# Kernel optimization log

Hardware: AMD Instinct MI355X
Metric: run time of the kernel (lower is better)

Reference implementation:

```python
import jax, jax.numpy as jnp
import numpy as np

NUM_USERS = 50000
NUM_ITEMS = 40000
EMB = 64
NNZ = 2_000_000
BATCH = 1024


def setup_inputs() -> dict:
    key = jax.random.key(0)
    ks = jax.random.split(key, 10)
    graph_rows = jax.random.randint(ks[0], (NNZ,), 0, NUM_USERS, dtype=jnp.int32)
    graph_cols = jax.random.randint(ks[1], (NNZ,), 0, NUM_ITEMS, dtype=jnp.int32)
    graph_vals = jax.random.uniform(ks[2], (NNZ,), dtype=jnp.float32)
    Wq = jax.random.normal(ks[3], (2 * EMB, NUM_ITEMS), dtype=jnp.float32) * 0.01
    bq = jnp.zeros((2 * EMB,), jnp.float32)
    Wp = jax.random.normal(ks[4], (NUM_ITEMS, EMB), dtype=jnp.float32) * 0.01
    bp = jnp.zeros((NUM_ITEMS,), jnp.float32)
    user = jax.random.randint(ks[5], (BATCH,), 0, NUM_USERS, dtype=jnp.int32)
    x = (jax.random.uniform(ks[6], (BATCH, NUM_ITEMS)) < 0.02).astype(jnp.float32)
    eps = jax.random.normal(ks[7], (NUM_USERS, EMB), dtype=jnp.float32)
    return dict(graph_vals=graph_vals, Wq=Wq, bq=bq, Wp=Wp, bp=bp, x=x,
                eps=eps, graph_rows=graph_rows, graph_cols=graph_cols, user=user)


def reference(graph_vals, Wq, bq, Wp, bp, x, eps, graph_rows, graph_cols, user):
    # ---- encode: single SpMM  h = Graph @ Wq^T + bq   (dropout off / eval mode)
    # gather item rows of Wq^T per nonzero, scale, scatter-add into users
    gathered = graph_vals[:, None] * Wq.T[graph_cols]          # [nnz, 2E]
    h = jax.ops.segment_sum(gathered, graph_rows, num_segments=NUM_USERS) + bq  # [U, 2E]
    mu, logvar = h[:, :EMB], h[:, EMB:]                        # [U, E] each
    # ---- reparameterize: z = mu + eps * exp(0.5*logvar)
    z = mu + eps * jnp.exp(0.5 * logvar)
    # ---- decode batch users: single Linear(E -> I)
    zb = z[user]                                               # [B, E]
    recon = zb @ Wp.T + bp                                     # [B, I]
    # ---- Mult-VAE ELBO (anneal = 1.0)
    log_sm = jax.nn.log_softmax(recon, axis=-1)
    recon_loss = -jnp.mean(jnp.sum(log_sm * x, axis=-1))
    mu_b, lv_b = mu[user], logvar[user]
    kl_loss = -0.5 * jnp.mean(jnp.sum(1.0 + lv_b - mu_b * mu_b - jnp.exp(lv_b), axis=-1))
    return jnp.stack([recon_loss, kl_loss])  # [2]: (recon_loss, KL_loss)
```

## Files before the change

kernel.cpp:

```cpp
#include <hip/hip_runtime.h>
#include <cstdint>

#define NUM_USERS 50000
#define NUM_ITEMS 40000
#define EMB 64
#define NNZ_E 2000000
#define BATCH 1024
#define NCH 625
#define CAP 131072
#define INF_I 0x7fffffff

typedef __attribute__((ext_vector_type(8))) short short8;
typedef __attribute__((ext_vector_type(4))) float float4v;

__device__ __forceinline__ unsigned short f2bf(float f) {
    union { float f; unsigned u; } x; x.f = f;
    unsigned r = x.u + 0x7fffu + ((x.u >> 16) & 1u);
    return (unsigned short)(r >> 16);
}
__device__ __forceinline__ float bf2f(unsigned short s) {
    return __uint_as_float(((unsigned)s) << 16);
}

__global__ void k_init(int* __restrict__ map, int* __restrict__ cnt, float* __restrict__ scal) {
    int t = blockIdx.x * blockDim.x + threadIdx.x;
    if (t < NUM_USERS) map[t] = INF_I;
    if (t < BATCH) cnt[t] = 0;
    if (t < 4) scal[t] = 0.f;
}

__global__ void k_map(const int* __restrict__ user, int* __restrict__ map) {
    int i = blockIdx.x * blockDim.x + threadIdx.x;
    if (i < BATCH) atomicMin(&map[user[i]], i);
}

__global__ __launch_bounds__(256) void k_prep(const float* __restrict__ Wq,
                                              const float* __restrict__ Wp,
                                              const int* __restrict__ rows,
                                              const int* __restrict__ map,
                                              unsigned short* __restrict__ WqT,
                                              unsigned short* __restrict__ WpBf,
                                              int* __restrict__ cnt) {
    __shared__ float t[128][33];
    const int bid = blockIdx.x;
    const int tid = threadIdx.x;
    if (bid < 1250) {
        const int jb = bid * 32;
        for (int idx = tid; idx < 4096; idx += 256) {
            int d = idx >> 5, c = idx & 31;
            t[d][c] = Wq[(size_t)d * NUM_ITEMS + jb + c];
        }
        __syncthreads();
        for (int idx = tid; idx < 4096; idx += 256) {
            int j = idx >> 7, d = idx & 127;
            WqT[(size_t)(jb + j) * 128 + d] = f2bf(t[d][j]);
        }
    } else if (bid < 3750) {
        const int e0 = ((bid - 1250) * 256 + tid) * 4;
        float4 w = *(const float4*)&Wp[e0];
        ushort4 o;
        o.x = f2bf(w.x); o.y = f2bf(w.y); o.z = f2bf(w.z); o.w = f2bf(w.w);
        *(ushort4*)&WpBf[e0] = o;
    } else {
        const int e = (bid - 3750) * 256 + tid;
        if (e < NNZ_E) {
            int s = map[rows[e]];
            if (s != INF_I) atomicAdd(&cnt[s], 1);
        }
    }
}

__global__ __launch_bounds__(1024) void k_scan(const int* __restrict__ cnt,
                                               int* __restrict__ off, int* __restrict__ cur) {
    __shared__ int s[1024];
    const int t = threadIdx.x;
    const int c = cnt[t];
    s[t] = c; __syncthreads();
    for (int d = 1; d < 1024; d <<= 1) {
        int v = (t >= d) ? s[t - d] : 0;
        __syncthreads();
        s[t] += v;
        __syncthreads();
    }
    int inc = s[t];
    off[t + 1] = inc;
    cur[t] = inc - c;
    if (t == 0) off[0] = 0;
}

__global__ __launch_bounds__(256) void k_scatter(const int* __restrict__ rows,
                                                 const int* __restrict__ cols,
                                                 const float* __restrict__ vals,
                                                 const int* __restrict__ map,
                                                 int* __restrict__ cur,
                                                 int2* __restrict__ compact) {
    const int e = blockIdx.x * 256 + threadIdx.x;
    if (e >= NNZ_E) return;
    int s = map[rows[e]];
    if (s == INF_I) return;
    int pos = atomicAdd(&cur[s], 1);
    if (pos < CAP) compact[pos] = make_int2(cols[e], __float_as_int(vals[e]));
}

__global__ __launch_bounds__(128) void k_hz(const int* __restrict__ user,
                                            const int* __restrict__ map,
                                            const int* __restrict__ off,
                                            const int2* __restrict__ compact,
                                            const unsigned short* __restrict__ WqT,
                                            const float* __restrict__ bq,
                                            const float* __restrict__ eps,
                                            unsigned short* __restrict__ zbBf,
                                            float* __restrict__ scal) {
    __shared__ float sh[128];
    const int i = blockIdx.x;
    const int tid = threadIdx.x;
    const int u = user[i];
    const int s = map[u];
    const int b = off[s], eN = off[s + 1];
    float acc = 0.f;
    int e = b;
    int2 cv = (e < eN) ? compact[e] : make_int2(0, 0);
    while (e < eN) {
        int2 nx = (e + 1 < eN) ? compact[e + 1] : make_int2(0, 0);
        float w = bf2f(WqT[(size_t)cv.x * 128 + tid]);
        acc = fmaf(__int_as_float(cv.y), w, acc);
        cv = nx; e++;
    }
    sh[tid] = acc + bq[tid];
    __syncthreads();
    if (tid < 64) {
        float mu = sh[tid];
        float lv = sh[tid + 64];
        float z = mu + eps[(size_t)u * EMB + tid] * __expf(0.5f * lv);
        zbBf[i * EMB + tid] = f2bf(z);
        float kl = 1.0f + lv - mu * mu - __expf(lv);
        #pragma unroll
        for (int o = 32; o; o >>= 1) kl += __shfl_down(kl, o);
        if (tid == 0) atomicAdd(&scal[1], kl);
    }
}

__global__ __launch_bounds__(256) void k_gemm(const unsigned short* __restrict__ zbBf,
                                              const unsigned short* __restrict__ WpBf,
                                              const float* __restrict__ bp,
                                              const float* __restrict__ x,
                                              float* __restrict__ part) {
    const int tid = threadIdx.x;
    const int wid = tid >> 6, lane = tid & 63;
    const int l15 = lane & 15, quad = lane >> 4;
    const int jb = blockIdx.x * 64;
    const int ibase = blockIdx.y * 128 + wid * 32;

    short8 af[2][2], bf[4][2];
    #pragma unroll
    for (int mt = 0; mt < 2; mt++) {
        const unsigned short* pa = zbBf + (size_t)(ibase + mt * 16 + l15) * EMB + quad * 8;
        af[mt][0] = *(const short8*)pa;
        af[mt][1] = *(const short8*)(pa + 32);
    }
    #pragma unroll
    for (int nt = 0; nt < 4; nt++) {
        const unsigned short* pb = WpBf + (size_t)(jb + nt * 16 + l15) * EMB + quad * 8;
        bf[nt][0] = *(const short8*)pb;
        bf[nt][1] = *(const short8*)(pb + 32);
    }
    float4v acc[2][4];
    #pragma unroll
    for (int mt = 0; mt < 2; mt++)
        #pragma unroll
        for (int nt = 0; nt < 4; nt++)
            acc[mt][nt] = (float4v){0.f, 0.f, 0.f, 0.f};
    #pragma unroll
    for (int kh = 0; kh < 2; kh++)
        #pragma unroll
        for (int mt = 0; mt < 2; mt++)
            #pragma unroll
            for (int nt = 0; nt < 4; nt++)
                acc[mt][nt] = __builtin_amdgcn_mfma_f32_16x16x32_bf16(
                    af[mt][kh], bf[nt][kh], acc[mt][nt], 0, 0, 0);

    float bpv[4];
    #pragma unroll
    for (int nt = 0; nt < 4; nt++) bpv[nt] = bp[jb + nt * 16 + l15];

    #pragma unroll
    for (int mt = 0; mt < 2; mt++) {
        #pragma unroll
        for (int r = 0; r < 4; r++) {
            const int gi = ibase + mt * 16 + quad * 4 + r;
            float v[4];
            #pragma unroll
            for (int nt = 0; nt < 4; nt++) v[nt] = acc[mt][nt][r] + bpv[nt];
            float mm = fmaxf(fmaxf(v[0], v[1]), fmaxf(v[2], v[3]));
            #pragma unroll
            for (int d = 1; d < 16; d <<= 1) mm = fmaxf(mm, __shfl_xor(mm, d));
            const float* xr = x + (size_t)gi * NUM_ITEMS + jb + l15;
            float s = 0.f, dx = 0.f, sx = 0.f;
            #pragma unroll
            for (int nt = 0; nt < 4; nt++) {
                float xv = xr[nt * 16];
                s += __expf(v[nt] - mm);
                dx = fmaf(v[nt], xv, dx);
                sx += xv;
            }
            #pragma unroll
            for (int d = 1; d < 16; d <<= 1) {
                s += __shfl_xor(s, d);
                dx += __shfl_xor(dx, d);
                sx += __shfl_xor(sx, d);
            }
            if (l15 == 0)
                *(float4*)&part[((size_t)gi * NCH + blockIdx.x) * 4] =
                    make_float4(mm, s, dx, sx);
        }
    }
}

__global__ __launch_bounds__(64) void k_merge(const float* __restrict__ part,
                                              float* __restrict__ scal) {
    const int row = blockIdx.x;
    const int lane = threadIdx.x;
    float M = -1e30f, S = 0.f, DX = 0.f, SX = 0.f;
    for (int c = lane; c < NCH; c += 64) {
        float4 p = *(const float4*)&part[((size_t)row * NCH + c) * 4];
        float M2 = fmaxf(M, p.x);
        S = S * __expf(M - M2) + p.y * __expf(p.x - M2);
        M = M2; DX += p.z; SX += p.w;
    }
    #pragma unroll
    for (int d = 1; d < 64; d <<= 1) {
        float M2  = __shfl_xor(M, d);
        float S2  = __shfl_xor(S, d);
        float DX2 = __shfl_xor(DX, d);
        float SX2 = __shfl_xor(SX, d);
        float Mn = fmaxf(M, M2);
        S = S * __expf(M - Mn) + S2 * __expf(M2 - Mn);
        M = Mn; DX += DX2; SX += SX2;
    }
    if (lane == 0) {
        float loss = DX - (M + logf(S)) * SX;
        atomicAdd(&scal[0], loss);
    }
}

__global__ void k_final(const float* __restrict__ scal, float* __restrict__ out) {
    if (threadIdx.x == 0 && blockIdx.x == 0) {
        out[0] = -scal[0] * (1.0f / BATCH);
        out[1] = -0.5f * scal[1] * (1.0f / BATCH);
    }
}

extern "C" void kernel_launch(void* const* d_in, const int* in_sizes, int n_in,
                              void* d_out, int out_size, void* d_ws, size_t ws_size,
                              hipStream_t stream) {
    const float* Wq         = (const float*)d_in[1];
    const float* bq         = (const float*)d_in[2];
    const float* Wp         = (const float*)d_in[3];
    const float* bp         = (const float*)d_in[4];
    const float* x          = (const float*)d_in[5];
    const float* eps        = (const float*)d_in[6];
    const float* graph_vals = (const float*)d_in[0];
    const int*   graph_rows = (const int*)d_in[7];
    const int*   graph_cols = (const int*)d_in[8];
    const int*   user       = (const int*)d_in[9];
    float* out = (float*)d_out;

    char* ws = (char*)d_ws;
    int*            map     = (int*)(ws + 0);
    int*            cnt     = (int*)(ws + 200704);
    int*            off     = (int*)(ws + 204800);
    int*            cur     = (int*)(ws + 209408);
    float*          scal    = (float*)(ws + 213504);
    int2*           compact = (int2*)(ws + 213520);
    unsigned short* zbBf    = (unsigned short*)(ws + 1262096);
    unsigned short* WpBf    = (unsigned short*)(ws + 1393168);
    unsigned short* WqT     = (unsigned short*)(ws + 6513168);
    float*          part    = (float*)(ws + 6513168);

    k_init<<<196, 256, 0, stream>>>(map, cnt, scal);
    k_map<<<4, 256, 0, stream>>>(user, map);
    k_prep<<<11563, 256, 0, stream>>>(Wq, Wp, graph_rows, map, WqT, WpBf, cnt);
    k_scan<<<1, 1024, 0, stream>>>(cnt, off, cur);
    k_scatter<<<7813, 256, 0, stream>>>(graph_rows, graph_cols, graph_vals, map, cur, compact);
    k_hz<<<BATCH, 128, 0, stream>>>(user, map, off, compact, WqT, bq, eps, zbBf, scal);
    dim3 g(NCH, BATCH / 128);
    k_gemm<<<g, 256, 0, stream>>>(zbBf, WpBf, bp, x, part);
    k_merge<<<BATCH, 64, 0, stream>>>(part, scal);
    k_final<<<1, 64, 0, stream>>>(scal, out);
}
```

Before: 391.3 us.

## Split x-dot term into sparse kernel and loop gemm over five column tiles

The dot of logits with x is rewritten algebraically as z·(sum of selected Wp rows) plus the sum of selected bp, computed in a new per-row kernel that scans x once and gathers only the nonzero columns. The GEMM kernel no longer reads x: it handles five 64-column tiles per block with an online max/sum-exp, and writes only (max, sum) partials to a five-times-smaller buffer. This removes strided x reads from the GEMM epilogue. In exchange it adds another full read of x, a shared-memory atomic list capped at 2048 entries, and a dot term built from bf16 Wp and fp32 z, so its rounding differs from the original logits.

```diff
diff --git a/kernel.cpp b/kernel.cpp
--- a/kernel.cpp
+++ b/kernel.cpp
@@ -6,7 +6,7 @@
 #define EMB 64
 #define NNZ_E 2000000
 #define BATCH 1024
-#define NCH 625
+#define NCHB 125
 #define CAP 131072
 #define INF_I 0x7fffffff
 
@@ -110,6 +110,7 @@
                                             const float* __restrict__ bq,
                                             const float* __restrict__ eps,
                                             unsigned short* __restrict__ zbBf,
+                                            float* __restrict__ zbF,
                                             float* __restrict__ scal) {
     __shared__ float sh[128];
     const int i = blockIdx.x;
@@ -133,6 +134,7 @@
         float lv = sh[tid + 64];
         float z = mu + eps[(size_t)u * EMB + tid] * __expf(0.5f * lv);
         zbBf[i * EMB + tid] = f2bf(z);
+        zbF[i * EMB + tid] = z;
         float kl = 1.0f + lv - mu * mu - __expf(lv);
         #pragma unroll
         for (int o = 32; o; o >>= 1) kl += __shfl_down(kl, o);
@@ -143,102 +145,172 @@
 __global__ __launch_bounds__(256) void k_gemm(const unsigned short* __restrict__ zbBf,
                                               const unsigned short* __restrict__ WpBf,
                                               const float* __restrict__ bp,
-                                              const float* __restrict__ x,
-                                              float* __restrict__ part) {
+                                              float2* __restrict__ part) {
     const int tid = threadIdx.x;
     const int wid = tid >> 6, lane = tid & 63;
     const int l15 = lane & 15, quad = lane >> 4;
-    const int jb = blockIdx.x * 64;
     const int ibase = blockIdx.y * 128 + wid * 32;
 
-    short8 af[2][2], bf[4][2];
+    short8 af[2][2];
     #pragma unroll
     for (int mt = 0; mt < 2; mt++) {
         const unsigned short* pa = zbBf + (size_t)(ibase + mt * 16 + l15) * EMB + quad * 8;
         af[mt][0] = *(const short8*)pa;
         af[mt][1] = *(const short8*)(pa + 32);
     }
-    #pragma unroll
-    for (int nt = 0; nt < 4; nt++) {
-        const unsigned short* pb = WpBf + (size_t)(jb + nt * 16 + l15) * EMB + quad * 8;
-        bf[nt][0] = *(const short8*)pb;
-        bf[nt][1] = *(const short8*)(pb + 32);
-    }
-    float4v acc[2][4];
+
+    float m_run[2][4], s_run[2][4];
     #pragma unroll
     for (int mt = 0; mt < 2; mt++)
         #pragma unroll
-        for (int nt = 0; nt < 4; nt++)
-            acc[mt][nt] = (float4v){0.f, 0.f, 0.f, 0.f};
-    #pragma unroll
-    for (int kh = 0; kh < 2; kh++)
+        for (int r = 0; r < 4; r++) { m_run[mt][r] = -1e30f; s_run[mt][r] = 0.f; }
+
+    #pragma unroll
+    for (int c5 = 0; c5 < 5; c5++) {
+        const int jb = blockIdx.x * 320 + c5 * 64;
+        short8 bfr[4][2];
+        #pragma unroll
+        for (int nt = 0; nt < 4; nt++) {
+            const unsigned short* pb = WpBf + (size_t)(jb + nt * 16 + l15) * EMB + quad * 8;
+            bfr[nt][0] = *(const short8*)pb;
+            bfr[nt][1] = *(const short8*)(pb + 32);
+        }
+        float4v acc[2][4];
         #pragma unroll
         for (int mt = 0; mt < 2; mt++)
             #pragma unroll
             for (int nt = 0; nt < 4; nt++)
-                acc[mt][nt] = __builtin_amdgcn_mfma_f32_16x16x32_bf16(
-                    af[mt][kh], bf[nt][kh], acc[mt][nt], 0, 0, 0);
-
-    float bpv[4];
-    #pragma unroll
-    for (int nt = 0; nt < 4; nt++) bpv[nt] = bp[jb + nt * 16 + l15];
-
-    #pragma unroll
-    for (int mt = 0; mt < 2; mt++) {
-        #pragma unroll
-        for (int r = 0; r < 4; r++) {
-            const int gi = ibase + mt * 16 + quad * 4 + r;
-            float v[4];
-            #pragma unroll
-            for (int nt = 0; nt < 4; nt++) v[nt] = acc[mt][nt][r] + bpv[nt];
-            float mm = fmaxf(fmaxf(v[0], v[1]), fmaxf(v[2], v[3]));
-            #pragma unroll
-            for (int d = 1; d < 16; d <<= 1) mm = fmaxf(mm, __shfl_xor(mm, d));
-            const float* xr = x + (size_t)gi * NUM_ITEMS + jb + l15;
-            float s = 0.f, dx = 0.f, sx = 0.f;
-            #pragma unroll
-            for (int nt = 0; nt < 4; nt++) {
-                float xv = xr[nt * 16];
-                s += __expf(v[nt] - mm);
-                dx = fmaf(v[nt], xv, dx);
-                sx += xv;
+                acc[mt][nt] = (float4v){0.f, 0.f, 0.f, 0.f};
+        #pragma unroll
+        for (int kh = 0; kh < 2; kh++)
+            #pragma unroll
+            for (int mt = 0; mt < 2; mt++)
+                #pragma unroll
+                for (int nt = 0; nt < 4; nt++)
+                    acc[mt][nt] = __builtin_amdgcn_mfma_f32_16x16x32_bf16(
+                        af[mt][kh], bfr[nt][kh], acc[mt][nt], 0, 0, 0);
+        float bpv[4];
+        #pragma unroll
+        for (int nt = 0; nt < 4; nt++) bpv[nt] = bp[jb + nt * 16 + l15];
+        #pragma unroll
+        for (int mt = 0; mt < 2; mt++) {
+            #pragma unroll
+            for (int r = 0; r < 4; r++) {
+                float v0 = acc[mt][0][r] + bpv[0];
+                float v1 = acc[mt][1][r] + bpv[1];
+                float v2 = acc[mt][2][r] + bpv[2];
+                float v3 = acc[mt][3][r] + bpv[3];
+                float mx = fmaxf(fmaxf(v0, v1), fmaxf(v2, v3));
+                float M2 = fmaxf(m_run[mt][r], mx);
+                float ls = __expf(v0 - M2) + __expf(v1 - M2) +
+                           __expf(v2 - M2) + __expf(v3 - M2);
+                s_run[mt][r] = s_run[mt][r] * __expf(m_run[mt][r] - M2) + ls;
+                m_run[mt][r] = M2;
             }
-            #pragma unroll
-            for (int d = 1; d < 16; d <<= 1) {
-                s += __shfl_xor(s, d);
-                dx += __shfl_xor(dx, d);
-                sx += __shfl_xor(sx, d);
+        }
+    }
+    #pragma unroll
+    for (int d = 1; d < 16; d <<= 1) {
+        #pragma unroll
+        for (int mt = 0; mt < 2; mt++)
+            #pragma unroll
+            for (int r = 0; r < 4; r++) {
+                float m2 = __shfl_xor(m_run[mt][r], d);
+                float s2 = __shfl_xor(s_run[mt][r], d);
+                float M = fmaxf(m_run[mt][r], m2);
+                s_run[mt][r] = s_run[mt][r] * __expf(m_run[mt][r] - M)
+                             + s2 * __expf(m2 - M);
+                m_run[mt][r] = M;
             }
-            if (l15 == 0)
-                *(float4*)&part[((size_t)gi * NCH + blockIdx.x) * 4] =
-                    make_float4(mm, s, dx, sx);
-        }
-    }
-}
-
-__global__ __launch_bounds__(64) void k_merge(const float* __restrict__ part,
+    }
+    if (l15 == 0) {
+        #pragma unroll
+        for (int mt = 0; mt < 2; mt++)
+            #pragma unroll
+            for (int r = 0; r < 4; r++) {
+                const int gi = ibase + mt * 16 + quad * 4 + r;
+                part[(size_t)gi * NCHB + blockIdx.x] =
+                    make_float2(m_run[mt][r], s_run[mt][r]);
+            }
+    }
+}
+
+__global__ __launch_bounds__(256) void k_x(const float* __restrict__ x,
+                                           const float* __restrict__ bp,
+                                           const unsigned short* __restrict__ WpBf,
+                                           const float* __restrict__ zbF,
+                                           float2* __restrict__ dxsx) {
+    __shared__ int list[2048];
+    __shared__ int lcnt;
+    __shared__ float redf[256];
+    __shared__ float redb[256];
+    __shared__ float redg[4][64];
+    const int i = blockIdx.x;
+    const int tid = threadIdx.x;
+    if (tid == 0) lcnt = 0;
+    __syncthreads();
+    float sxl = 0.f, sbl = 0.f;
+    const float4* xr = (const float4*)(x + (size_t)i * NUM_ITEMS);
+    for (int idx = tid; idx < NUM_ITEMS / 4; idx += 256) {
+        float4 v = xr[idx];
+        float vv[4] = {v.x, v.y, v.z, v.w};
+        #pragma unroll
+        for (int e = 0; e < 4; e++) {
+            if (vv[e] != 0.f) {
+                int col = idx * 4 + e;
+                int p = atomicAdd(&lcnt, 1);
+                if (p < 2048) list[p] = col;
+                sxl += vv[e];
+                sbl += bp[col];
+            }
+        }
+    }
+    redf[tid] = sxl; redb[tid] = sbl;
+    __syncthreads();
+    for (int d = 128; d; d >>= 1) {
+        if (tid < d) { redf[tid] += redf[tid + d]; redb[tid] += redb[tid + d]; }
+        __syncthreads();
+    }
+    const int nnz = min(lcnt, 2048);
+    const int grp = tid >> 6, dim = tid & 63;
+    float acc = 0.f;
+    for (int e = grp; e < nnz; e += 4)
+        acc += bf2f(WpBf[(size_t)list[e] * EMB + dim]);
+    redg[grp][dim] = acc;
+    __syncthreads();
+    if (tid < 64) {
+        float sv = redg[0][tid] + redg[1][tid] + redg[2][tid] + redg[3][tid];
+        float d = sv * zbF[(size_t)i * EMB + tid];
+        #pragma unroll
+        for (int o = 32; o; o >>= 1) d += __shfl_down(d, o);
+        if (tid == 0) dxsx[i] = make_float2(d + redb[0], redf[0]);
+    }
+}
+
+__global__ __launch_bounds__(64) void k_merge(const float2* __restrict__ part,
+                                              const float2* __restrict__ dxsx,
                                               float* __restrict__ scal) {
     const int row = blockIdx.x;
     const int lane = threadIdx.x;
-    float M = -1e30f, S = 0.f, DX = 0.f, SX = 0.f;
-    for (int c = lane; c < NCH; c += 64) {
-        float4 p = *(const float4*)&part[((size_t)row * NCH + c) * 4];
+    float M = -1e30f, S = 0.f;
+    for (int c = lane; c < NCHB; c += 64) {
+        float2 p = part[(size_t)row * NCHB + c];
         float M2 = fmaxf(M, p.x);
         S = S * __expf(M - M2) + p.y * __expf(p.x - M2);
-        M = M2; DX += p.z; SX += p.w;
+        M = M2;
     }
     #pragma unroll
     for (int d = 1; d < 64; d <<= 1) {
-        float M2  = __shfl_xor(M, d);
-        float S2  = __shfl_xor(S, d);
-        float DX2 = __shfl_xor(DX, d);
-        float SX2 = __shfl_xor(SX, d);
+        float M2 = __shfl_xor(M, d);
+        float S2 = __shfl_xor(S, d);
         float Mn = fmaxf(M, M2);
         S = S * __expf(M - Mn) + S2 * __expf(M2 - Mn);
-        M = Mn; DX += DX2; SX += SX2;
+        M = Mn;
     }
     if (lane == 0) {
-        float loss = DX - (M + logf(S)) * SX;
+        float lse = M + logf(S);
+        float2 ds = dxsx[row];
+        float loss = ds.x - lse * ds.y;
         atomicAdd(&scal[0], loss);
     }
 }
@@ -253,13 +325,13 @@
 extern "C" void kernel_launch(void* const* d_in, const int* in_sizes, int n_in,
                               void* d_out, int out_size, void* d_ws, size_t ws_size,
                               hipStream_t stream) {
+    const float* graph_vals = (const float*)d_in[0];
     const float* Wq         = (const float*)d_in[1];
     const float* bq         = (const float*)d_in[2];
     const float* Wp         = (const float*)d_in[3];
     const float* bp         = (const float*)d_in[4];
     const float* x          = (const float*)d_in[5];
     const float* eps        = (const float*)d_in[6];
-    const float* graph_vals = (const float*)d_in[0];
     const int*   graph_rows = (const int*)d_in[7];
     const int*   graph_cols = (const int*)d_in[8];
     const int*   user       = (const int*)d_in[9];
@@ -273,18 +345,21 @@
     float*          scal    = (float*)(ws + 213504);
     int2*           compact = (int2*)(ws + 213520);
     unsigned short* zbBf    = (unsigned short*)(ws + 1262096);
-    unsigned short* WpBf    = (unsigned short*)(ws + 1393168);
-    unsigned short* WqT     = (unsigned short*)(ws + 6513168);
-    float*          part    = (float*)(ws + 6513168);
+    float*          zbF     = (float*)(ws + 1393168);
+    float2*         dxsx    = (float2*)(ws + 1655312);
+    unsigned short* WpBf    = (unsigned short*)(ws + 1663504);
+    unsigned short* WqT     = (unsigned short*)(ws + 6783504);
+    float2*         part    = (float2*)(ws + 6783504);
 
     k_init<<<196, 256, 0, stream>>>(map, cnt, scal);
     k_map<<<4, 256, 0, stream>>>(user, map);
     k_prep<<<11563, 256, 0, stream>>>(Wq, Wp, graph_rows, map, WqT, WpBf, cnt);
     k_scan<<<1, 1024, 0, stream>>>(cnt, off, cur);
     k_scatter<<<7813, 256, 0, stream>>>(graph_rows, graph_cols, graph_vals, map, cur, compact);
-    k_hz<<<BATCH, 128, 0, stream>>>(user, map, off, compact, WqT, bq, eps, zbBf, scal);
-    dim3 g(NCH, BATCH / 128);
-    k_gemm<<<g, 256, 0, stream>>>(zbBf, WpBf, bp, x, part);
-    k_merge<<<BATCH, 64, 0, stream>>>(part, scal);
+    k_hz<<<BATCH, 128, 0, stream>>>(user, map, off, compact, WqT, bq, eps, zbBf, zbF, scal);
+    dim3 g(NCHB, BATCH / 128);
+    k_gemm<<<g, 256, 0, stream>>>(zbBf, WpBf, bp, part);
+    k_x<<<BATCH, 256, 0, stream>>>(x, bp, WpBf, zbF, dxsx);
+    k_merge<<<BATCH, 64, 0, stream>>>(part, dxsx, scal);
     k_final<<<1, 64, 0, stream>>>(scal, out);
 }
```

Measured after the change: 508.1 us. 1.3x slower.
